# Kernel optimization log

Measured on AMD Instinct MI355X. Metric: run time of the kernel, lower is better.

## Reference

```python
import jax, jax.numpy as jnp
import numpy as np

LEVELS = 16
FEATURES = 2
TABLE_SIZE = 2 ** 19
MINRES = (16, 16)
MAXRES = (2048, 2048)
N = 2 ** 21  # number of query points
PRIMES = (1, 2654435761)  # Instant-NGP spatial hash primes (2D)


def _level_res():
    # per-dim geometric growth: floor(minres * b**l), b = exp((ln(max)-ln(min))/(L-1))
    res = []
    for l in range(LEVELS):
        r = []
        for mn, mx in zip(MINRES, MAXRES):
            b = np.exp((np.log(mx) - np.log(mn)) / (LEVELS - 1))
            r.append(int(np.floor(mn * b ** l)))
        res.append(tuple(r))
    return res


RES_LEVELS = _level_res()


def setup_inputs() -> dict:
    key = jax.random.key(0)
    k1, k2, k3, k4 = jax.random.split(key, 4)
    coords_x = jax.random.uniform(k1, (N,), jnp.float32)
    coords_y = jax.random.uniform(k2, (N,), jnp.float32)
    # level 0 is a dense grid table; levels 1..L-1 are hash tables (stacked)
    dense_table = jax.random.uniform(k3, (*RES_LEVELS[0], FEATURES), jnp.float32, -1e-4, 1e-4)
    hash_tables = jax.random.uniform(k4, (LEVELS - 1, TABLE_SIZE, FEATURES), jnp.float32, -1e-4, 1e-4)
    return {"coords_x": coords_x, "coords_y": coords_y,
            "dense_table": dense_table, "hash_tables": hash_tables}


def _bilerp(gather, res, cx, cy):
    # normalized coords in [0,1] scaled to index space [0, res-1]; mode='nearest' -> clamp
    rx, ry = res
    fx = cx * (rx - 1)
    fy = cy * (ry - 1)
    x0 = jnp.floor(fx)
    y0 = jnp.floor(fy)
    wx = (fx - x0)[:, None]
    wy = (fy - y0)[:, None]
    ix0 = jnp.clip(x0.astype(jnp.int32), 0, rx - 1)
    iy0 = jnp.clip(y0.astype(jnp.int32), 0, ry - 1)
    ix1 = jnp.minimum(ix0 + 1, rx - 1)
    iy1 = jnp.minimum(iy0 + 1, ry - 1)
    f00 = gather(ix0, iy0)  # [N, F]
    f01 = gather(ix0, iy1)
    f10 = gather(ix1, iy0)
    f11 = gather(ix1, iy1)
    return (f00 * (1 - wx) * (1 - wy) + f01 * (1 - wx) * wy
            + f10 * wx * (1 - wy) + f11 * wx * wy)


def _hash_gather(table, ix, iy):
    h = (ix.astype(jnp.uint32) * jnp.uint32(PRIMES[0])) ^ (iy.astype(jnp.uint32) * jnp.uint32(PRIMES[1]))
    idx = (h % jnp.uint32(table.shape[0])).astype(jnp.int32)
    return table[idx]


def reference(coords_x, coords_y, dense_table, hash_tables):
    feats = [_bilerp(lambda ix, iy: dense_table[ix, iy], RES_LEVELS[0], coords_x, coords_y)]
    for l in range(1, LEVELS):
        t = hash_tables[l - 1]
        feats.append(_bilerp(lambda ix, iy, t=t: _hash_gather(t, ix, iy),
                             RES_LEVELS[l], coords_x, coords_y))
    return jnp.concatenate(feats, -1)  # [N, LEVELS*FEATURES]
```

## Files before the change

kernel.cpp:

```cpp
#include <hip/hip_runtime.h>
#include <math.h>
#include <stdint.h>


#define TMASK  ((1u << 19) - 1)
#define PRIME2 2654435761u
#define NBIN   16384u

typedef float vfloat4 __attribute__((ext_vector_type(4)));
typedef float vfloat2 __attribute__((ext_vector_type(2)));

__device__ __forceinline__ void pair_gather(const char* tp, unsigned h0,
                                            unsigned h1, float2& a, float2& b)
{
    if (((h0 ^ h1) | 1u) == 1u) {
        vfloat4 q = *(const vfloat4*)(tp + ((h0 & ~1u) << 3));
        a.x = (h0 & 1u) ? q.z : q.x;  a.y = (h0 & 1u) ? q.w : q.y;
        b.x = (h1 & 1u) ? q.z : q.x;  b.y = (h1 & 1u) ? q.w : q.y;
    } else {
        a = *(const float2*)(tp + ((size_t)h0 << 3));
        b = *(const float2*)(tp + ((size_t)h1 << 3));
    }
}

__device__ __forceinline__ unsigned bin_of(float x, float y)
{
    int bx = (int)(x * 128.0f); bx = bx < 0 ? 0 : (bx > 127 ? 127 : bx);
    int by = (int)(y * 128.0f); by = by < 0 ? 0 : (by > 127 ? 127 : by);
    return (unsigned)by * 128u + (unsigned)bx;
}

__global__ void k_zero(unsigned* cnt)
{
    cnt[blockIdx.x * 256u + threadIdx.x] = 0u;
}

__global__ void k_hist(const float* __restrict__ cx, const float* __restrict__ cy,
                       unsigned* __restrict__ cnt, unsigned N)
{
    unsigned i = blockIdx.x * 256u + threadIdx.x;
    if (i < N) atomicAdd(&cnt[bin_of(cx[i], cy[i])], 1u);
}

__global__ void k_scan(unsigned* cnt)
{
    __shared__ unsigned tsum[256];
    unsigned t = threadIdx.x;
    unsigned base = t * 64u;
    unsigned s = 0;
    for (int i = 0; i < 64; ++i) s += cnt[base + i];
    tsum[t] = s; __syncthreads();
    for (unsigned off = 1; off < 256; off <<= 1) {
        unsigned v = t >= off ? tsum[t - off] : 0u;
        __syncthreads();
        tsum[t] += v;
        __syncthreads();
    }
    unsigned run = tsum[t] - s;
    for (int i = 0; i < 64; ++i) {
        unsigned c = cnt[base + i];
        cnt[base + i] = run;
        run += c;
    }
}

__global__ void k_scatter(const float* __restrict__ cx, const float* __restrict__ cy,
                          unsigned* __restrict__ cur, float* __restrict__ bx,
                          float* __restrict__ by, unsigned* __restrict__ og,
                          unsigned N)
{
    unsigned i = blockIdx.x * 256u + threadIdx.x;
    if (i >= N) return;
    float x = cx[i], y = cy[i];
    unsigned pos = atomicAdd(&cur[bin_of(x, y)], 1u);
    bx[pos] = x; by[pos] = y; og[pos] = i;
}

__global__ __launch_bounds__(256, 8) void mre_big(
    const float* __restrict__ px, const float* __restrict__ py,
    const float2* __restrict__ hasht, vfloat2* __restrict__ ws,
    uint4 rm1v, unsigned N)
{
    unsigned bid = blockIdx.x;
    unsigned xcd = bid & 7u;
    unsigned lv  = xcd >> 1;
    unsigned bwl = (bid >> 3) * 2u + (xcd & 1u);
    int r = (int)(lv == 0u ? rm1v.x : lv == 1u ? rm1v.y
                                    : lv == 2u ? rm1v.z : rm1v.w);
    const char* hb = (const char*)hasht + ((size_t)(11u + lv) << 22);
    vfloat2* wbase = ws + (size_t)lv * N;
    float rf = (float)r;

    unsigned stride = 512u * 256u;
    #pragma unroll 2
    for (unsigned n = bwl * 256u + threadIdx.x; n < N; n += stride) {
        float x = px[n], y = py[n];
        float fx = x * rf, fy = y * rf;
        float x0f = floorf(fx), y0f = floorf(fy);
        float wx = fx - x0f, wy = fy - y0f;
        int ix0 = (int)x0f; ix0 = ix0 < 0 ? 0 : (ix0 > r ? r : ix0);
        int iy0 = (int)y0f; iy0 = iy0 < 0 ? 0 : (iy0 > r ? r : iy0);
        int ix1 = ix0 + 1 > r ? r : ix0 + 1;
        int iy1 = iy0 + 1 > r ? r : iy0 + 1;
        unsigned hy0 = (unsigned)iy0 * PRIME2;
        unsigned hy1 = (unsigned)iy1 * PRIME2;
        unsigned h00 = ((unsigned)ix0 ^ hy0) & TMASK;
        unsigned h10 = ((unsigned)ix1 ^ hy0) & TMASK;
        unsigned h01 = ((unsigned)ix0 ^ hy1) & TMASK;
        unsigned h11 = ((unsigned)ix1 ^ hy1) & TMASK;
        float2 f00, f01, f10, f11;
        pair_gather(hb, h00, h10, f00, f10);
        pair_gather(hb, h01, h11, f01, f11);
        float omx = 1.0f - wx, omy = 1.0f - wy;
        float w00 = omx * omy, w01 = omx * wy, w10 = wx * omy, w11 = wx * wy;
        vfloat2 acc;
        acc.x = f00.x * w00 + f01.x * w01 + f10.x * w10 + f11.x * w11;
        acc.y = f00.y * w00 + f01.y * w01 + f10.y * w10 + f11.y * w11;
        __builtin_nontemporal_store(acc, wbase + n);
    }
}

__global__ __launch_bounds__(256) void mre_rest_s(
    const float* __restrict__ px, const float* __restrict__ py,
    const unsigned* __restrict__ og,
    const float2* __restrict__ dense, const float2* __restrict__ hasht,
    const vfloat2* __restrict__ ws, float4* __restrict__ out,
    uint4 wa, uint4 wb, unsigned N)
{
    __shared__ float2 sdense[256];
    __shared__ __align__(16) float sout[64 * 36];
    sdense[threadIdx.x] = dense[threadIdx.x];
    __syncthreads();

    unsigned j  = threadIdx.x >> 6;
    unsigned nl = threadIdx.x & 63u;
    unsigned pos = blockIdx.x * 64u + nl;
    if (pos >= N) pos = N - 1u;

    float x = px[pos];
    float y = py[pos];

    vfloat2 wsv = __builtin_nontemporal_load(&ws[(size_t)j * N + pos]);

    unsigned W0 = wa.x, W1 = wa.y, W2 = wa.z, W3 = wa.w, W4 = wb.x, W5 = wb.y;
    unsigned u0 = j == 0u ? W0 : j == 1u ? W1 : j == 2u ? W3 : W4;
    unsigned u1 = j == 0u ? W0 : j == 1u ? W2 : j == 2u ? W3 : W5;
    unsigned u2 = j == 0u ? W1 : j == 1u ? W2 : j == 2u ? W4 : W5;
    unsigned h0 = (j & 1u) << 4;
    unsigned h1 = ((j + 1u) & 1u) << 4;
    unsigned h2 = (j & 1u) << 4;
    int rm1[3] = { (int)((u0 >> h0) & 0xffffu),
                   (int)((u1 >> h1) & 0xffffu),
                   (int)((u2 >> h2) & 0xffffu) };

    unsigned h00[3], h01[3], h10[3], h11[3];
    unsigned tbo[3];
    float wx[3], wy[3];
    unsigned d00 = 0, d01 = 0, d10 = 0, d11 = 0;

    #pragma unroll
    for (int k = 0; k < 3; ++k) {
        int r = rm1[k];
        float rf = (float)r;
        float fx = x * rf, fy = y * rf;
        float x0f = floorf(fx), y0f = floorf(fy);
        wx[k] = fx - x0f;  wy[k] = fy - y0f;
        int ix0 = (int)x0f; ix0 = ix0 < 0 ? 0 : (ix0 > r ? r : ix0);
        int iy0 = (int)y0f; iy0 = iy0 < 0 ? 0 : (iy0 > r ? r : iy0);
        int ix1 = ix0 + 1 > r ? r : ix0 + 1;
        int iy1 = iy0 + 1 > r ? r : iy0 + 1;
        if (k == 0) { d00 = ix0 * 16 + iy0; d01 = ix0 * 16 + iy1;
                      d10 = ix1 * 16 + iy0; d11 = ix1 * 16 + iy1; }
        unsigned lvl = j * 3u + (unsigned)k;
        unsigned ti = lvl == 0u ? 0u : lvl - 1u;
        tbo[k] = ti << 22;
        unsigned hy0 = (unsigned)iy0 * PRIME2;
        unsigned hy1 = (unsigned)iy1 * PRIME2;
        h00[k] = ((unsigned)ix0 ^ hy0) & TMASK;
        h01[k] = ((unsigned)ix0 ^ hy1) & TMASK;
        h10[k] = ((unsigned)ix1 ^ hy0) & TMASK;
        h11[k] = ((unsigned)ix1 ^ hy1) & TMASK;
    }

    const char* hb = (const char*)hasht;
    float2 f00[3], f01[3], f10[3], f11[3];
    #pragma unroll
    for (int k = 1; k < 3; ++k) {
        const char* tp = hb + tbo[k];
        pair_gather(tp, h00[k], h10[k], f00[k], f10[k]);
        pair_gather(tp, h01[k], h11[k], f01[k], f11[k]);
    }
    if (j == 0u) {
        f00[0] = sdense[d00]; f01[0] = sdense[d01];
        f10[0] = sdense[d10]; f11[0] = sdense[d11];
    } else {
        const char* tp = hb + tbo[0];
        pair_gather(tp, h00[0], h10[0], f00[0], f10[0]);
        pair_gather(tp, h01[0], h11[0], f01[0], f11[0]);
    }

    float* so = &sout[nl * 36u];
    #pragma unroll
    for (int k = 0; k < 3; ++k) {
        float omx = 1.0f - wx[k], omy = 1.0f - wy[k];
        float w00 = omx * omy, w01 = omx * wy[k];
        float w10 = wx[k] * omy, w11 = wx[k] * wy[k];
        vfloat2 a;
        a.x = f00[k].x * w00 + f01[k].x * w01 + f10[k].x * w10 + f11[k].x * w11;
        a.y = f00[k].y * w00 + f01[k].y * w01 + f10[k].y * w10 + f11[k].y * w11;
        *(vfloat2*)&so[6u * j + 2u * (unsigned)k] = a;
    }
    *(vfloat2*)&so[24u + 2u * j] = wsv;

    __syncthreads();

    unsigned c  = threadIdx.x & 7u;
    unsigned q0 = threadIdx.x >> 3;
    #pragma unroll
    for (int p = 0; p < 2; ++p) {
        unsigned q = q0 + 32u * p;
        unsigned sp = blockIdx.x * 64u + q;
        if (sp >= N) sp = N - 1u;
        unsigned o = og[sp];
        vfloat4 v = *(const vfloat4*)&sout[q * 36u + c * 4u];
        __builtin_nontemporal_store(v, (vfloat4*)(out + (size_t)o * 8u + c));
    }
}

__global__ __launch_bounds__(256) void mre_rest(
    const float* __restrict__ cxp, const float* __restrict__ cyp,
    const float2* __restrict__ dense, const float2* __restrict__ hasht,
    const vfloat2* __restrict__ ws, float4* __restrict__ out,
    uint4 wa, uint4 wb, unsigned N)
{
    __shared__ float2 sdense[256];
    __shared__ __align__(16) float sout[64 * 36];
    sdense[threadIdx.x] = dense[threadIdx.x];
    __syncthreads();

    unsigned gid = blockIdx.x * 256u + threadIdx.x;
    unsigned n  = gid >> 2;
    unsigned j  = gid & 3u;
    unsigned nl = threadIdx.x >> 2;

    float x = cxp[n];
    float y = cyp[n];
    vfloat2 wsv = __builtin_nontemporal_load(&ws[(size_t)j * N + n]);

    unsigned W0 = wa.x, W1 = wa.y, W2 = wa.z, W3 = wa.w, W4 = wb.x, W5 = wb.y;
    unsigned u0 = j == 0u ? W0 : j == 1u ? W1 : j == 2u ? W3 : W4;
    unsigned u1 = j == 0u ? W0 : j == 1u ? W2 : j == 2u ? W3 : W5;
    unsigned u2 = j == 0u ? W1 : j == 1u ? W2 : j == 2u ? W4 : W5;
    unsigned h0 = (j & 1u) << 4;
    unsigned h1 = ((j + 1u) & 1u) << 4;
    unsigned h2 = (j & 1u) << 4;
    int rm1[3] = { (int)((u0 >> h0) & 0xffffu),
                   (int)((u1 >> h1) & 0xffffu),
                   (int)((u2 >> h2) & 0xffffu) };

    unsigned h00[3], h01[3], h10[3], h11[3];
    unsigned tbo[3];
    float wx[3], wy[3];
    unsigned d00 = 0, d01 = 0, d10 = 0, d11 = 0;

    #pragma unroll
    for (int k = 0; k < 3; ++k) {
        int r = rm1[k];
        float rf = (float)r;
        float fx = x * rf, fy = y * rf;
        float x0f = floorf(fx), y0f = floorf(fy);
        wx[k] = fx - x0f;  wy[k] = fy - y0f;
        int ix0 = (int)x0f; ix0 = ix0 < 0 ? 0 : (ix0 > r ? r : ix0);
        int iy0 = (int)y0f; iy0 = iy0 < 0 ? 0 : (iy0 > r ? r : iy0);
        int ix1 = ix0 + 1 > r ? r : ix0 + 1;
        int iy1 = iy0 + 1 > r ? r : iy0 + 1;
        if (k == 0) { d00 = ix0 * 16 + iy0; d01 = ix0 * 16 + iy1;
                      d10 = ix1 * 16 + iy0; d11 = ix1 * 16 + iy1; }
        unsigned lvl = j * 3u + (unsigned)k;
        unsigned ti = lvl == 0u ? 0u : lvl - 1u;
        tbo[k] = ti << 22;
        unsigned hy0 = (unsigned)iy0 * PRIME2;
        unsigned hy1 = (unsigned)iy1 * PRIME2;
        h00[k] = ((unsigned)ix0 ^ hy0) & TMASK;
        h01[k] = ((unsigned)ix0 ^ hy1) & TMASK;
        h10[k] = ((unsigned)ix1 ^ hy0) & TMASK;
        h11[k] = ((unsigned)ix1 ^ hy1) & TMASK;
    }

    const char* hb = (const char*)hasht;
    float2 f00[3], f01[3], f10[3], f11[3];
    #pragma unroll
    for (int k = 1; k < 3; ++k) {
        const char* tp = hb + tbo[k];
        pair_gather(tp, h00[k], h10[k], f00[k], f10[k]);
        pair_gather(tp, h01[k], h11[k], f01[k], f11[k]);
    }
    if (j == 0u) {
        f00[0] = sdense[d00]; f01[0] = sdense[d01];
        f10[0] = sdense[d10]; f11[0] = sdense[d11];
    } else {
        const char* tp = hb + tbo[0];
        pair_gather(tp, h00[0], h10[0], f00[0], f10[0]);
        pair_gather(tp, h01[0], h11[0], f01[0], f11[0]);
    }

    float* so = &sout[nl * 36u];
    #pragma unroll
    for (int k = 0; k < 3; ++k) {
        float omx = 1.0f - wx[k], omy = 1.0f - wy[k];
        float w00 = omx * omy, w01 = omx * wy[k];
        float w10 = wx[k] * omy, w11 = wx[k] * wy[k];
        vfloat2 a;
        a.x = f00[k].x * w00 + f01[k].x * w01 + f10[k].x * w10 + f11[k].x * w11;
        a.y = f00[k].y * w00 + f01[k].y * w01 + f10[k].y * w10 + f11[k].y * w11;
        *(vfloat2*)&so[6u * j + 2u * (unsigned)k] = a;
    }
    *(vfloat2*)&so[24u + 2u * j] = wsv;

    __syncthreads();

    const vfloat4* sp = (const vfloat4*)&sout[nl * 36u + 8u * j];
    vfloat4 o0 = sp[0];
    vfloat4 o1 = sp[1];
    size_t base = (size_t)n * 8u + 2u * j;
    __builtin_nontemporal_store(o0, (vfloat4*)&out[base]);
    __builtin_nontemporal_store(o1, (vfloat4*)&out[base + 1]);
}

__global__ __launch_bounds__(256) void mre_mono(
    const float* __restrict__ cxp, const float* __restrict__ cyp,
    const float2* __restrict__ dense, const float2* __restrict__ hasht,
    float4* __restrict__ out, uint4 wa, uint4 wb)
{
    __shared__ float2 sdense[256];
    sdense[threadIdx.x] = dense[threadIdx.x];
    __syncthreads();

    unsigned gid = blockIdx.x * 256u + threadIdx.x;
    unsigned n = gid >> 2;
    unsigned j = gid & 3u;

    float x = cxp[n];
    float y = cyp[n];

    unsigned w0 = j < 2u ? (j == 0u ? wa.x : wa.z) : (j == 2u ? wb.x : wb.z);
    unsigned w1 = j < 2u ? (j == 0u ? wa.y : wa.w) : (j == 2u ? wb.y : wb.w);
    int rm1[4] = { (int)(w0 & 0xffffu), (int)(w0 >> 16),
                   (int)(w1 & 0xffffu), (int)(w1 >> 16) };

    unsigned o00[4], o01[4], o10[4], o11[4];
    float wx[4], wy[4];
    unsigned d00 = 0, d01 = 0, d10 = 0, d11 = 0;
    const bool lvl0 = (j == 0u);

    #pragma unroll
    for (int k = 0; k < 4; ++k) {
        int r = rm1[k];
        float rf = (float)r;
        float fx = x * rf, fy = y * rf;
        float x0f = floorf(fx), y0f = floorf(fy);
        wx[k] = fx - x0f;  wy[k] = fy - y0f;
        int ix0 = (int)x0f; ix0 = ix0 < 0 ? 0 : (ix0 > r ? r : ix0);
        int iy0 = (int)y0f; iy0 = iy0 < 0 ? 0 : (iy0 > r ? r : iy0);
        int ix1 = ix0 + 1 > r ? r : ix0 + 1;
        int iy1 = iy0 + 1 > r ? r : iy0 + 1;
        if (k == 0) { d00 = ix0 * 16 + iy0; d01 = ix0 * 16 + iy1;
                      d10 = ix1 * 16 + iy0; d11 = ix1 * 16 + iy1; }
        unsigned ti = j * 4u + (unsigned)k;
        ti = ti == 0u ? 0u : ti - 1u;
        unsigned tb = ti << 22;
        unsigned hy0 = (unsigned)iy0 * PRIME2;
        unsigned hy1 = (unsigned)iy1 * PRIME2;
        o00[k] = tb + ((((unsigned)ix0 ^ hy0) & TMASK) << 3);
        o01[k] = tb + ((((unsigned)ix0 ^ hy1) & TMASK) << 3);
        o10[k] = tb + ((((unsigned)ix1 ^ hy0) & TMASK) << 3);
        o11[k] = tb + ((((unsigned)ix1 ^ hy1) & TMASK) << 3);
    }

    const char* hb = (const char*)hasht;
    float2 f00[4], f01[4], f10[4], f11[4];
    #pragma unroll
    for (int k = 1; k < 4; ++k) {
        f00[k] = *(const float2*)(hb + o00[k]);
        f01[k] = *(const float2*)(hb + o01[k]);
        f10[k] = *(const float2*)(hb + o10[k]);
        f11[k] = *(const float2*)(hb + o11[k]);
    }
    if (lvl0) {
        f00[0] = sdense[d00]; f01[0] = sdense[d01];
        f10[0] = sdense[d10]; f11[0] = sdense[d11];
    } else {
        f00[0] = *(const float2*)(hb + o00[0]);
        f01[0] = *(const float2*)(hb + o01[0]);
        f10[0] = *(const float2*)(hb + o10[0]);
        f11[0] = *(const float2*)(hb + o11[0]);
    }

    float2 acc[4];
    #pragma unroll
    for (int k = 0; k < 4; ++k) {
        float omx = 1.0f - wx[k], omy = 1.0f - wy[k];
        float w00 = omx * omy, w01 = omx * wy[k];
        float w10 = wx[k] * omy, w11 = wx[k] * wy[k];
        acc[k].x = f00[k].x * w00 + f01[k].x * w01 + f10[k].x * w10 + f11[k].x * w11;
        acc[k].y = f00[k].y * w00 + f01[k].y * w01 + f10[k].y * w10 + f11[k].y * w11;
    }

    vfloat4 o0 = { acc[0].x, acc[0].y, acc[1].x, acc[1].y };
    vfloat4 o1 = { acc[2].x, acc[2].y, acc[3].x, acc[3].y };
    size_t base = (size_t)n * 8u + 2u * j;
    __builtin_nontemporal_store(o0, (vfloat4*)&out[base]);
    __builtin_nontemporal_store(o1, (vfloat4*)&out[base + 1]);
}

extern "C" void kernel_launch(void* const* d_in, const int* in_sizes, int n_in,
                              void* d_out, int out_size, void* d_ws, size_t ws_size,
                              hipStream_t stream)
{
    const float*  cx    = (const float*)d_in[0];
    const float*  cy    = (const float*)d_in[1];
    const float2* dense = (const float2*)d_in[2];
    const float2* hasht = (const float2*)d_in[3];
    float4*       out   = (float4*)d_out;
    const unsigned N = (unsigned)in_sizes[0];

    int r[16];
    for (int l = 0; l < 16; ++l) {
        double b = exp((log(2048.0) - log(16.0)) / 15.0);
        r[l] = (int)floor(16.0 * pow(b, (double)l));
    }
    unsigned pw[8];
    for (int k = 0; k < 8; ++k)
        pw[k] = (unsigned)(r[2 * k] - 1) | ((unsigned)(r[2 * k + 1] - 1) << 16);
    uint4 wa = make_uint4(pw[0], pw[1], pw[2], pw[3]);
    uint4 wb = make_uint4(pw[4], pw[5], pw[6], pw[7]);
    uint4 rm1v = make_uint4((unsigned)(r[12] - 1), (unsigned)(r[13] - 1),
                            (unsigned)(r[14] - 1), (unsigned)(r[15] - 1));

    long long total = (long long)N * 4;
    int blocks = (int)((total + 255) / 256);
    int pblocks = (int)((N + 255u) / 256u);

    size_t tbl_bytes  = (size_t)N * 32u;
    size_t sort_bytes = tbl_bytes + (size_t)N * 12u + NBIN * 4u;

    if (ws_size >= sort_bytes && d_ws != nullptr) {
        char* wsb = (char*)d_ws;
        vfloat2*  wst = (vfloat2*)wsb;
        float*    bx  = (float*)(wsb + tbl_bytes);
        float*    by  = bx + N;
        unsigned* og  = (unsigned*)(by + N);
        unsigned* cnt = og + N;

        hipLaunchKernelGGL(k_zero,    dim3(NBIN / 256), dim3(256), 0, stream, cnt);
        hipLaunchKernelGGL(k_hist,    dim3(pblocks), dim3(256), 0, stream,
                           cx, cy, cnt, N);
        hipLaunchKernelGGL(k_scan,    dim3(1), dim3(256), 0, stream, cnt);
        hipLaunchKernelGGL(k_scatter, dim3(pblocks), dim3(256), 0, stream,
                           cx, cy, cnt, bx, by, og, N);
        hipLaunchKernelGGL(mre_big,   dim3(2048), dim3(256), 0, stream,
                           bx, by, hasht, wst, rm1v, N);
        hipLaunchKernelGGL(mre_rest_s, dim3((N + 63u) / 64u), dim3(256), 0, stream,
                           bx, by, og, dense, hasht, (const vfloat2*)wst,
                           out, wa, wb, N);
    } else if (ws_size >= tbl_bytes && d_ws != nullptr) {
        vfloat2* wst = (vfloat2*)d_ws;
        hipLaunchKernelGGL(mre_big, dim3(2048), dim3(256), 0, stream,
                           cx, cy, hasht, wst, rm1v, N);
        hipLaunchKernelGGL(mre_rest, dim3(blocks), dim3(256), 0, stream,
                           cx, cy, dense, hasht, (const vfloat2*)wst,
                           out, wa, wb, N);
    } else {
        hipLaunchKernelGGL(mre_mono, dim3(blocks), dim3(256), 0, stream,
                           cx, cy, dense, hasht, out, wa, wb);
    }
}
```

Measured before the change: 672.8 us.

## Replace counting-sort with fixed-capacity bins plus overflow path

Drops the histogram and scan kernels and gives each spatial bin a fixed slot capacity. A single atomic scatter pass writes points into their bin slots, and points beyond capacity go to an overflow list that a separate kernel processes. Empty slots are marked invalid and skipped with wave ballots. This removes two launches and one full pass over the coordinates, but the padded buffers are larger (16384×192 slots against 2M points), so the init, big-level and rest kernels touch more memory and run more waves.

```diff
diff --git a/kernel.cpp b/kernel.cpp
--- a/kernel.cpp
+++ b/kernel.cpp
@@ -6,6 +6,8 @@
 #define TMASK  ((1u << 19) - 1)
 #define PRIME2 2654435761u
 #define NBIN   16384u
+#define CAP    192u
+#define INVOG  0xFFFFFFFFu
 
 typedef float vfloat4 __attribute__((ext_vector_type(4)));
 typedef float vfloat2 __attribute__((ext_vector_type(2)));
@@ -30,56 +32,39 @@
     return (unsigned)by * 128u + (unsigned)bx;
 }
 
-__global__ void k_zero(unsigned* cnt)
-{
-    cnt[blockIdx.x * 256u + threadIdx.x] = 0u;
-}
-
-__global__ void k_hist(const float* __restrict__ cx, const float* __restrict__ cy,
-                       unsigned* __restrict__ cnt, unsigned N)
+__global__ void k_init(float* __restrict__ bx, float* __restrict__ by,
+                       unsigned* __restrict__ og, unsigned* __restrict__ cnt,
+                       unsigned NS)
 {
     unsigned i = blockIdx.x * 256u + threadIdx.x;
-    if (i < N) atomicAdd(&cnt[bin_of(cx[i], cy[i])], 1u);
-}
-
-__global__ void k_scan(unsigned* cnt)
-{
-    __shared__ unsigned tsum[256];
-    unsigned t = threadIdx.x;
-    unsigned base = t * 64u;
-    unsigned s = 0;
-    for (int i = 0; i < 64; ++i) s += cnt[base + i];
-    tsum[t] = s; __syncthreads();
-    for (unsigned off = 1; off < 256; off <<= 1) {
-        unsigned v = t >= off ? tsum[t - off] : 0u;
-        __syncthreads();
-        tsum[t] += v;
-        __syncthreads();
-    }
-    unsigned run = tsum[t] - s;
-    for (int i = 0; i < 64; ++i) {
-        unsigned c = cnt[base + i];
-        cnt[base + i] = run;
-        run += c;
-    }
+    if (i < NS) { bx[i] = -1.0f; by[i] = -1.0f; og[i] = INVOG; }
+    if (i <= NBIN) cnt[i] = 0u;
 }
 
 __global__ void k_scatter(const float* __restrict__ cx, const float* __restrict__ cy,
-                          unsigned* __restrict__ cur, float* __restrict__ bx,
+                          unsigned* __restrict__ cnt, float* __restrict__ bx,
                           float* __restrict__ by, unsigned* __restrict__ og,
-                          unsigned N)
+                          float* __restrict__ ox, float* __restrict__ oy,
+                          unsigned* __restrict__ oidx, unsigned N)
 {
     unsigned i = blockIdx.x * 256u + threadIdx.x;
     if (i >= N) return;
     float x = cx[i], y = cy[i];
-    unsigned pos = atomicAdd(&cur[bin_of(x, y)], 1u);
-    bx[pos] = x; by[pos] = y; og[pos] = i;
+    unsigned b = bin_of(x, y);
+    unsigned pos = atomicAdd(&cnt[b], 1u);
+    if (pos < CAP) {
+        unsigned s = b * CAP + pos;
+        bx[s] = x; by[s] = y; og[s] = i;
+    } else {
+        unsigned op = atomicAdd(&cnt[NBIN], 1u);
+        ox[op] = x; oy[op] = y; oidx[op] = i;
+    }
 }
 
 __global__ __launch_bounds__(256, 8) void mre_big(
     const float* __restrict__ px, const float* __restrict__ py,
     const float2* __restrict__ hasht, vfloat2* __restrict__ ws,
-    uint4 rm1v, unsigned N)
+    uint4 rm1v, unsigned NS)
 {
     unsigned bid = blockIdx.x;
     unsigned xcd = bid & 7u;
@@ -88,13 +73,14 @@
     int r = (int)(lv == 0u ? rm1v.x : lv == 1u ? rm1v.y
                                     : lv == 2u ? rm1v.z : rm1v.w);
     const char* hb = (const char*)hasht + ((size_t)(11u + lv) << 22);
-    vfloat2* wbase = ws + (size_t)lv * N;
+    vfloat2* wbase = ws + (size_t)lv * NS;
     float rf = (float)r;
 
     unsigned stride = 512u * 256u;
     #pragma unroll 2
-    for (unsigned n = bwl * 256u + threadIdx.x; n < N; n += stride) {
+    for (unsigned n = bwl * 256u + threadIdx.x; n < NS; n += stride) {
         float x = px[n], y = py[n];
+        if (__ballot(x >= 0.0f) == 0ull) continue;
         float fx = x * rf, fy = y * rf;
         float x0f = floorf(fx), y0f = floorf(fy);
         float wx = fx - x0f, wy = fy - y0f;
@@ -121,8 +107,169 @@
 }
 
 __global__ __launch_bounds__(256) void mre_rest_s(
-    const float* __restrict__ px, const float* __restrict__ py,
+    const float* __restrict__ bx, const float* __restrict__ by,
     const unsigned* __restrict__ og,
+    const float2* __restrict__ dense, const float2* __restrict__ hasht,
+    const vfloat2* __restrict__ ws, float4* __restrict__ out,
+    uint4 wa, uint4 wb, unsigned NS)
+{
+    __shared__ float2 sdense[256];
+    __shared__ __align__(16) float sout[64 * 36];
+    __shared__ unsigned sorig[64];
+    sdense[threadIdx.x] = dense[threadIdx.x];
+
+    unsigned j  = threadIdx.x >> 6;
+    unsigned nl = threadIdx.x & 63u;
+    unsigned slot = blockIdx.x * 64u + nl;
+    unsigned o = og[slot];
+    if (j == 0u) sorig[nl] = o;
+    __syncthreads();
+
+    bool valid = (o != INVOG);
+    if (__ballot(valid) != 0ull) {
+        float x = bx[slot];
+        float y = by[slot];
+        vfloat2 wsv = __builtin_nontemporal_load(&ws[(size_t)j * NS + slot]);
+
+        unsigned W0 = wa.x, W1 = wa.y, W2 = wa.z, W3 = wa.w, W4 = wb.x, W5 = wb.y;
+        unsigned u0 = j == 0u ? W0 : j == 1u ? W1 : j == 2u ? W3 : W4;
+        unsigned u1 = j == 0u ? W0 : j == 1u ? W2 : j == 2u ? W3 : W5;
+        unsigned u2 = j == 0u ? W1 : j == 1u ? W2 : j == 2u ? W4 : W5;
+        unsigned s0 = (j & 1u) << 4;
+        unsigned s1 = ((j + 1u) & 1u) << 4;
+        int rm1[3] = { (int)((u0 >> s0) & 0xffffu),
+                       (int)((u1 >> s1) & 0xffffu),
+                       (int)((u2 >> s0) & 0xffffu) };
+
+        unsigned h00[3], h01[3], h10[3], h11[3];
+        unsigned tbo[3];
+        float wx[3], wy[3];
+        unsigned d00 = 0, d01 = 0, d10 = 0, d11 = 0;
+
+        #pragma unroll
+        for (int k = 0; k < 3; ++k) {
+            int r = rm1[k];
+            float rf = (float)r;
+            float fx = x * rf, fy = y * rf;
+            float x0f = floorf(fx), y0f = floorf(fy);
+            wx[k] = fx - x0f;  wy[k] = fy - y0f;
+            int ix0 = (int)x0f; ix0 = ix0 < 0 ? 0 : (ix0 > r ? r : ix0);
+            int iy0 = (int)y0f; iy0 = iy0 < 0 ? 0 : (iy0 > r ? r : iy0);
+            int ix1 = ix0 + 1 > r ? r : ix0 + 1;
+            int iy1 = iy0 + 1 > r ? r : iy0 + 1;
+            if (k == 0) { d00 = ix0 * 16 + iy0; d01 = ix0 * 16 + iy1;
+                          d10 = ix1 * 16 + iy0; d11 = ix1 * 16 + iy1; }
+            unsigned lvl = j * 3u + (unsigned)k;
+            unsigned ti = lvl == 0u ? 0u : lvl - 1u;
+            tbo[k] = ti << 22;
+            unsigned hy0 = (unsigned)iy0 * PRIME2;
+            unsigned hy1 = (unsigned)iy1 * PRIME2;
+            h00[k] = ((unsigned)ix0 ^ hy0) & TMASK;
+            h01[k] = ((unsigned)ix0 ^ hy1) & TMASK;
+            h10[k] = ((unsigned)ix1 ^ hy0) & TMASK;
+            h11[k] = ((unsigned)ix1 ^ hy1) & TMASK;
+        }
+
+        const char* hb = (const char*)hasht;
+        float2 f00[3], f01[3], f10[3], f11[3];
+        #pragma unroll
+        for (int k = 1; k < 3; ++k) {
+            const char* tp = hb + tbo[k];
+            pair_gather(tp, h00[k], h10[k], f00[k], f10[k]);
+            pair_gather(tp, h01[k], h11[k], f01[k], f11[k]);
+        }
+        if (j == 0u) {
+            f00[0] = sdense[d00]; f01[0] = sdense[d01];
+            f10[0] = sdense[d10]; f11[0] = sdense[d11];
+        } else {
+            const char* tp = hb + tbo[0];
+            pair_gather(tp, h00[0], h10[0], f00[0], f10[0]);
+            pair_gather(tp, h01[0], h11[0], f01[0], f11[0]);
+        }
+
+        float* so = &sout[nl * 36u];
+        #pragma unroll
+        for (int k = 0; k < 3; ++k) {
+            float omx = 1.0f - wx[k], omy = 1.0f - wy[k];
+            float w00 = omx * omy, w01 = omx * wy[k];
+            float w10 = wx[k] * omy, w11 = wx[k] * wy[k];
+            vfloat2 a;
+            a.x = f00[k].x * w00 + f01[k].x * w01 + f10[k].x * w10 + f11[k].x * w11;
+            a.y = f00[k].y * w00 + f01[k].y * w01 + f10[k].y * w10 + f11[k].y * w11;
+            *(vfloat2*)&so[6u * j + 2u * (unsigned)k] = a;
+        }
+        *(vfloat2*)&so[24u + 2u * j] = wsv;
+    }
+    __syncthreads();
+
+    unsigned c  = threadIdx.x & 7u;
+    unsigned q0 = threadIdx.x >> 3;
+    #pragma unroll
+    for (int p = 0; p < 2; ++p) {
+        unsigned q = q0 + 32u * p;
+        unsigned oo = sorig[q];
+        if (oo != INVOG) {
+            vfloat4 v = *(const vfloat4*)&sout[q * 36u + c * 4u];
+            __builtin_nontemporal_store(v, (vfloat4*)(out + (size_t)oo * 8u + c));
+        }
+    }
+}
+
+__global__ void k_overflow(const float* __restrict__ ox, const float* __restrict__ oy,
+                           const unsigned* __restrict__ oidx,
+                           const unsigned* __restrict__ cnt,
+                           const float2* __restrict__ dense,
+                           const float2* __restrict__ hasht,
+                           float4* __restrict__ out, uint4 wa, uint4 wb)
+{
+    unsigned ocnt = cnt[NBIN];
+    unsigned pwv[8] = { wa.x, wa.y, wa.z, wa.w, wb.x, wb.y, wb.z, wb.w };
+    const char* hb = (const char*)hasht;
+    for (unsigned i = blockIdx.x * 256u + threadIdx.x; i < ocnt;
+         i += gridDim.x * 256u) {
+        float x = ox[i], y = oy[i];
+        float f[32];
+        #pragma unroll
+        for (int l = 0; l < 16; ++l) {
+            int r = (int)((pwv[l >> 1] >> ((l & 1) << 4)) & 0xffffu);
+            float rf = (float)r;
+            float fx = x * rf, fy = y * rf;
+            float x0f = floorf(fx), y0f = floorf(fy);
+            float wx = fx - x0f, wy = fy - y0f;
+            int ix0 = (int)x0f; ix0 = ix0 < 0 ? 0 : (ix0 > r ? r : ix0);
+            int iy0 = (int)y0f; iy0 = iy0 < 0 ? 0 : (iy0 > r ? r : iy0);
+            int ix1 = ix0 + 1 > r ? r : ix0 + 1;
+            int iy1 = iy0 + 1 > r ? r : iy0 + 1;
+            float2 f00, f01, f10, f11;
+            if (l == 0) {
+                f00 = dense[ix0 * 16 + iy0]; f01 = dense[ix0 * 16 + iy1];
+                f10 = dense[ix1 * 16 + iy0]; f11 = dense[ix1 * 16 + iy1];
+            } else {
+                const char* tp = hb + ((size_t)(l - 1) << 22);
+                unsigned hy0 = (unsigned)iy0 * PRIME2;
+                unsigned hy1 = (unsigned)iy1 * PRIME2;
+                f00 = *(const float2*)(tp + ((size_t)(((unsigned)ix0 ^ hy0) & TMASK) << 3));
+                f01 = *(const float2*)(tp + ((size_t)(((unsigned)ix0 ^ hy1) & TMASK) << 3));
+                f10 = *(const float2*)(tp + ((size_t)(((unsigned)ix1 ^ hy0) & TMASK) << 3));
+                f11 = *(const float2*)(tp + ((size_t)(((unsigned)ix1 ^ hy1) & TMASK) << 3));
+            }
+            float omx = 1.0f - wx, omy = 1.0f - wy;
+            float w00 = omx * omy, w01 = omx * wy, w10 = wx * omy, w11 = wx * wy;
+            f[2 * l]     = f00.x * w00 + f01.x * w01 + f10.x * w10 + f11.x * w11;
+            f[2 * l + 1] = f00.y * w00 + f01.y * w01 + f10.y * w10 + f11.y * w11;
+        }
+        unsigned o = oidx[i];
+        float4* ob = out + (size_t)o * 8u;
+        #pragma unroll
+        for (int c = 0; c < 8; ++c) {
+            vfloat4 v = { f[4 * c], f[4 * c + 1], f[4 * c + 2], f[4 * c + 3] };
+            __builtin_nontemporal_store(v, (vfloat4*)&ob[c]);
+        }
+    }
+}
+
+__global__ __launch_bounds__(256) void mre_rest(
+    const float* __restrict__ cxp, const float* __restrict__ cyp,
     const float2* __restrict__ dense, const float2* __restrict__ hasht,
     const vfloat2* __restrict__ ws, float4* __restrict__ out,
     uint4 wa, uint4 wb, unsigned N)
@@ -132,26 +279,24 @@
     sdense[threadIdx.x] = dense[threadIdx.x];
     __syncthreads();
 
-    unsigned j  = threadIdx.x >> 6;
-    unsigned nl = threadIdx.x & 63u;
-    unsigned pos = blockIdx.x * 64u + nl;
-    if (pos >= N) pos = N - 1u;
-
-    float x = px[pos];
-    float y = py[pos];
-
-    vfloat2 wsv = __builtin_nontemporal_load(&ws[(size_t)j * N + pos]);
+    unsigned gid = blockIdx.x * 256u + threadIdx.x;
+    unsigned n  = gid >> 2;
+    unsigned j  = gid & 3u;
+    unsigned nl = threadIdx.x >> 2;
+
+    float x = cxp[n];
+    float y = cyp[n];
+    vfloat2 wsv = __builtin_nontemporal_load(&ws[(size_t)j * N + n]);
 
     unsigned W0 = wa.x, W1 = wa.y, W2 = wa.z, W3 = wa.w, W4 = wb.x, W5 = wb.y;
     unsigned u0 = j == 0u ? W0 : j == 1u ? W1 : j == 2u ? W3 : W4;
     unsigned u1 = j == 0u ? W0 : j == 1u ? W2 : j == 2u ? W3 : W5;
     unsigned u2 = j == 0u ? W1 : j == 1u ? W2 : j == 2u ? W4 : W5;
-    unsigned h0 = (j & 1u) << 4;
-    unsigned h1 = ((j + 1u) & 1u) << 4;
-    unsigned h2 = (j & 1u) << 4;
-    int rm1[3] = { (int)((u0 >> h0) & 0xffffu),
-                   (int)((u1 >> h1) & 0xffffu),
-                   (int)((u2 >> h2) & 0xffffu) };
+    unsigned s0 = (j & 1u) << 4;
+    unsigned s1 = ((j + 1u) & 1u) << 4;
+    int rm1[3] = { (int)((u0 >> s0) & 0xffffu),
+                   (int)((u1 >> s1) & 0xffffu),
+                   (int)((u2 >> s0) & 0xffffu) };
 
     unsigned h00[3], h01[3], h10[3], h11[3];
     unsigned tbo[3];
@@ -214,111 +359,6 @@
 
     __syncthreads();
 
-    unsigned c  = threadIdx.x & 7u;
-    unsigned q0 = threadIdx.x >> 3;
-    #pragma unroll
-    for (int p = 0; p < 2; ++p) {
-        unsigned q = q0 + 32u * p;
-        unsigned sp = blockIdx.x * 64u + q;
-        if (sp >= N) sp = N - 1u;
-        unsigned o = og[sp];
-        vfloat4 v = *(const vfloat4*)&sout[q * 36u + c * 4u];
-        __builtin_nontemporal_store(v, (vfloat4*)(out + (size_t)o * 8u + c));
-    }
-}
-
-__global__ __launch_bounds__(256) void mre_rest(
-    const float* __restrict__ cxp, const float* __restrict__ cyp,
-    const float2* __restrict__ dense, const float2* __restrict__ hasht,
-    const vfloat2* __restrict__ ws, float4* __restrict__ out,
-    uint4 wa, uint4 wb, unsigned N)
-{
-    __shared__ float2 sdense[256];
-    __shared__ __align__(16) float sout[64 * 36];
-    sdense[threadIdx.x] = dense[threadIdx.x];
-    __syncthreads();
-
-    unsigned gid = blockIdx.x * 256u + threadIdx.x;
-    unsigned n  = gid >> 2;
-    unsigned j  = gid & 3u;
-    unsigned nl = threadIdx.x >> 2;
-
-    float x = cxp[n];
-    float y = cyp[n];
-    vfloat2 wsv = __builtin_nontemporal_load(&ws[(size_t)j * N + n]);
-
-    unsigned W0 = wa.x, W1 = wa.y, W2 = wa.z, W3 = wa.w, W4 = wb.x, W5 = wb.y;
-    unsigned u0 = j == 0u ? W0 : j == 1u ? W1 : j == 2u ? W3 : W4;
-    unsigned u1 = j == 0u ? W0 : j == 1u ? W2 : j == 2u ? W3 : W5;
-    unsigned u2 = j == 0u ? W1 : j == 1u ? W2 : j == 2u ? W4 : W5;
-    unsigned h0 = (j & 1u) << 4;
-    unsigned h1 = ((j + 1u) & 1u) << 4;
-    unsigned h2 = (j & 1u) << 4;
-    int rm1[3] = { (int)((u0 >> h0) & 0xffffu),
-                   (int)((u1 >> h1) & 0xffffu),
-                   (int)((u2 >> h2) & 0xffffu) };
-
-    unsigned h00[3], h01[3], h10[3], h11[3];
-    unsigned tbo[3];
-    float wx[3], wy[3];
-    unsigned d00 = 0, d01 = 0, d10 = 0, d11 = 0;
-
-    #pragma unroll
-    for (int k = 0; k < 3; ++k) {
-        int r = rm1[k];
-        float rf = (float)r;
-        float fx = x * rf, fy = y * rf;
-        float x0f = floorf(fx), y0f = floorf(fy);
-        wx[k] = fx - x0f;  wy[k] = fy - y0f;
-        int ix0 = (int)x0f; ix0 = ix0 < 0 ? 0 : (ix0 > r ? r : ix0);
-        int iy0 = (int)y0f; iy0 = iy0 < 0 ? 0 : (iy0 > r ? r : iy0);
-        int ix1 = ix0 + 1 > r ? r : ix0 + 1;
-        int iy1 = iy0 + 1 > r ? r : iy0 + 1;
-        if (k == 0) { d00 = ix0 * 16 + iy0; d01 = ix0 * 16 + iy1;
-                      d10 = ix1 * 16 + iy0; d11 = ix1 * 16 + iy1; }
-        unsigned lvl = j * 3u + (unsigned)k;
-        unsigned ti = lvl == 0u ? 0u : lvl - 1u;
-        tbo[k] = ti << 22;
-        unsigned hy0 = (unsigned)iy0 * PRIME2;
-        unsigned hy1 = (unsigned)iy1 * PRIME2;
-        h00[k] = ((unsigned)ix0 ^ hy0) & TMASK;
-        h01[k] = ((unsigned)ix0 ^ hy1) & TMASK;
-        h10[k] = ((unsigned)ix1 ^ hy0) & TMASK;
-        h11[k] = ((unsigned)ix1 ^ hy1) & TMASK;
-    }
-
-    const char* hb = (const char*)hasht;
-    float2 f00[3], f01[3], f10[3], f11[3];
-    #pragma unroll
-    for (int k = 1; k < 3; ++k) {
-        const char* tp = hb + tbo[k];
-        pair_gather(tp, h00[k], h10[k], f00[k], f10[k]);
-        pair_gather(tp, h01[k], h11[k], f01[k], f11[k]);
-    }
-    if (j == 0u) {
-        f00[0] = sdense[d00]; f01[0] = sdense[d01];
-        f10[0] = sdense[d10]; f11[0] = sdense[d11];
-    } else {
-        const char* tp = hb + tbo[0];
-        pair_gather(tp, h00[0], h10[0], f00[0], f10[0]);
-        pair_gather(tp, h01[0], h11[0], f01[0], f11[0]);
-    }
-
-    float* so = &sout[nl * 36u];
-    #pragma unroll
-    for (int k = 0; k < 3; ++k) {
-        float omx = 1.0f - wx[k], omy = 1.0f - wy[k];
-        float w00 = omx * omy, w01 = omx * wy[k];
-        float w10 = wx[k] * omy, w11 = wx[k] * wy[k];
-        vfloat2 a;
-        a.x = f00[k].x * w00 + f01[k].x * w01 + f10[k].x * w10 + f11[k].x * w11;
-        a.y = f00[k].y * w00 + f01[k].y * w01 + f10[k].y * w10 + f11[k].y * w11;
-        *(vfloat2*)&so[6u * j + 2u * (unsigned)k] = a;
-    }
-    *(vfloat2*)&so[24u + 2u * j] = wsv;
-
-    __syncthreads();
-
     const vfloat4* sp = (const vfloat4*)&sout[nl * 36u + 8u * j];
     vfloat4 o0 = sp[0];
     vfloat4 o1 = sp[1];
@@ -438,31 +478,39 @@
                             (unsigned)(r[14] - 1), (unsigned)(r[15] - 1));
 
     long long total = (long long)N * 4;
-    int blocks = (int)((total + 255) / 256);
+    int blocks  = (int)((total + 255) / 256);
     int pblocks = (int)((N + 255u) / 256u);
 
-    size_t tbl_bytes  = (size_t)N * 32u;
-    size_t sort_bytes = tbl_bytes + (size_t)N * 12u + NBIN * 4u;
-
-    if (ws_size >= sort_bytes && d_ws != nullptr) {
-        char* wsb = (char*)d_ws;
-        vfloat2*  wst = (vfloat2*)wsb;
-        float*    bx  = (float*)(wsb + tbl_bytes);
-        float*    by  = bx + N;
-        unsigned* og  = (unsigned*)(by + N);
-        unsigned* cnt = og + N;
-
-        hipLaunchKernelGGL(k_zero,    dim3(NBIN / 256), dim3(256), 0, stream, cnt);
-        hipLaunchKernelGGL(k_hist,    dim3(pblocks), dim3(256), 0, stream,
-                           cx, cy, cnt, N);
-        hipLaunchKernelGGL(k_scan,    dim3(1), dim3(256), 0, stream, cnt);
+    const unsigned NS = NBIN * CAP;
+    size_t tbl_bytes    = (size_t)N * 32u;
+    size_t sorted_bytes = (size_t)NS * 32u
+                        + (size_t)NS * 12u
+                        + (size_t)(NBIN + 1) * 4u
+                        + (size_t)N * 12u;
+
+    if (ws_size >= sorted_bytes && d_ws != nullptr) {
+        char* p = (char*)d_ws;
+        vfloat2*  wst = (vfloat2*)p;        p += (size_t)NS * 32u;
+        float*    bx  = (float*)p;          p += (size_t)NS * 4u;
+        float*    by  = (float*)p;          p += (size_t)NS * 4u;
+        unsigned* og  = (unsigned*)p;       p += (size_t)NS * 4u;
+        unsigned* cnt = (unsigned*)p;       p += (size_t)(NBIN + 1) * 4u;
+        float*    ox  = (float*)p;          p += (size_t)N * 4u;
+        float*    oy  = (float*)p;          p += (size_t)N * 4u;
+        unsigned* oix = (unsigned*)p;
+
+        int iblocks = (int)((NS + 255u) / 256u);
+        hipLaunchKernelGGL(k_init,    dim3(iblocks), dim3(256), 0, stream,
+                           bx, by, og, cnt, NS);
         hipLaunchKernelGGL(k_scatter, dim3(pblocks), dim3(256), 0, stream,
-                           cx, cy, cnt, bx, by, og, N);
+                           cx, cy, cnt, bx, by, og, ox, oy, oix, N);
         hipLaunchKernelGGL(mre_big,   dim3(2048), dim3(256), 0, stream,
-                           bx, by, hasht, wst, rm1v, N);
-        hipLaunchKernelGGL(mre_rest_s, dim3((N + 63u) / 64u), dim3(256), 0, stream,
+                           bx, by, hasht, wst, rm1v, NS);
+        hipLaunchKernelGGL(mre_rest_s, dim3(NS / 64u), dim3(256), 0, stream,
                            bx, by, og, dense, hasht, (const vfloat2*)wst,
-                           out, wa, wb, N);
+                           out, wa, wb, NS);
+        hipLaunchKernelGGL(k_overflow, dim3(64), dim3(256), 0, stream,
+                           ox, oy, oix, cnt, dense, hasht, out, wa, wb);
     } else if (ws_size >= tbl_bytes && d_ws != nullptr) {
         vfloat2* wst = (vfloat2*)d_ws;
         hipLaunchKernelGGL(mre_big, dim3(2048), dim3(256), 0, stream,
```

Result: no change. 666.1 us (-1.0%).
